# Kernel optimization log

Hardware: AMD Instinct MI355X
Metric: run time of the kernel (lower is better)

The kernel has to match this reference:

```python
import jax, jax.numpy as jnp
import numpy as np

B, S, H = 2, 2048, 2048
NH, NKV, HD = 16, 8, 128        # head_dim = H // NH
WINDOW = 1024                    # sliding window size
THETA = 100000.0                 # rope_theta (RotaryEmbedding base)


def setup_inputs() -> dict:
    key = jax.random.key(0)
    ks = jax.random.split(key, 5)
    hidden = jax.random.normal(ks[0], (B, S, H), jnp.float32)
    # fused QKV projection: [H, NH*HD + 2*NKV*HD]
    W_pack = jax.random.normal(ks[1], (H, NH * HD + 2 * NKV * HD), jnp.float32) * (H ** -0.5)
    W_o = jax.random.normal(ks[2], (NH * HD, H), jnp.float32) * ((NH * HD) ** -0.5)
    # per-KV-head 2-tap causal conv weights, softmax-normalized (as in nn.Parameter init)
    conv_k = jax.nn.softmax(jax.random.normal(ks[3], (NKV, 2), jnp.float32), axis=-1)
    conv_v = jax.nn.softmax(jax.random.normal(ks[4], (NKV, 2), jnp.float32), axis=-1)
    return {"hidden": hidden, "W_pack": W_pack, "W_o": W_o, "conv_k": conv_k, "conv_v": conv_v}


def _rope(x, cos, sin):
    # x: (b, s, h, d); cos/sin: (s, d//2); non-interleaved (rotate-half) form
    d2 = x.shape[-1] // 2
    x1, x2 = x[..., :d2], x[..., d2:]
    c = cos[None, :, None, :]
    s = sin[None, :, None, :]
    return jnp.concatenate([x1 * c - x2 * s, x2 * c + x1 * s], axis=-1)


def _causal_conv2(x, w):
    # x: (b, s, kv, d); w: (kv, 2). out[t] = w0*x[t-1] + w1*x[t], zero-padded at t=0
    x_prev = jnp.pad(x, ((0, 0), (1, 0), (0, 0), (0, 0)))[:, :-1]
    return w[None, None, :, 0:1] * x_prev + w[None, None, :, 1:2] * x


def reference(hidden, W_pack, W_o, conv_k, conv_v):
    b, s, _ = hidden.shape
    qkv = hidden @ W_pack                                  # (b, s, NH*HD + 2*NKV*HD)
    q = qkv[..., : NH * HD].reshape(b, s, NH, HD)
    k = qkv[..., NH * HD : NH * HD + NKV * HD].reshape(b, s, NKV, HD)
    v = qkv[..., NH * HD + NKV * HD :].reshape(b, s, NKV, HD)

    inv_freq = 1.0 / (THETA ** (jnp.arange(0, HD, 2, dtype=jnp.float32) / HD))
    freqs = jnp.outer(jnp.arange(s, dtype=jnp.float32), inv_freq)  # (s, HD/2)
    cos, sin = jnp.cos(freqs), jnp.sin(freqs)
    q = _rope(q, cos, sin)
    k = _rope(k, cos, sin)

    # learned 2-tap causal conv mixing adjacent K/V states, per KV head
    k = _causal_conv2(k, conv_k)
    v = _causal_conv2(v, conv_v)

    # GQA: repeat kv heads to match query heads
    group = NH // NKV
    k = jnp.repeat(k, group, axis=2)  # (b, s, NH, HD)
    v = jnp.repeat(v, group, axis=2)

    scores = jnp.einsum('bqhd,bkhd->bhqk', q, k) / jnp.sqrt(jnp.float32(HD))
    i = jnp.arange(s)[:, None]
    j = jnp.arange(s)[None, :]
    mask = (j <= i) & (i - j < WINDOW)  # causal sliding-window mask
    scores = jnp.where(mask[None, None], scores, jnp.finfo(scores.dtype).min)
    probs = jax.nn.softmax(scores, axis=-1)
    out = jnp.einsum('bhqk,bkhd->bqhd', probs, v).reshape(b, s, NH * HD)
    return out @ W_o
```

## Files before the change

kernel.cpp:

```cpp
#include <hip/hip_runtime.h>

#define DI __device__ __forceinline__

typedef unsigned short u16;
typedef __attribute__((ext_vector_type(8))) short s16x8;
typedef __attribute__((ext_vector_type(8))) unsigned short u16x8;
typedef __attribute__((ext_vector_type(4))) float f32x4;
typedef __attribute__((ext_vector_type(16))) float f32x16;

DI u16 f2bf(float x) {
  union { float f; unsigned u; } a; a.f = x;
  unsigned r = a.u + 0x7FFFu + ((a.u >> 16) & 1u);
  return (u16)(r >> 16);
}
DI float bf2f(u16 u) {
  union { unsigned u; float f; } a; a.u = ((unsigned)u) << 16;
  return a.f;
}
DI void gload16(const void* g, void* l) {
  __builtin_amdgcn_global_load_lds(
      (const __attribute__((address_space(1))) unsigned int*)g,
      (__attribute__((address_space(3))) unsigned int*)l, 16, 0, 0);
}
DI f32x4 mfma16(s16x8 a, s16x8 b, f32x4 c) {
  return __builtin_amdgcn_mfma_f32_16x16x32_bf16(a, b, c, 0, 0, 0);
}
DI f32x16 mfma32(s16x8 a, s16x8 b, f32x16 c) {
  return __builtin_amdgcn_mfma_f32_32x32x16_bf16(a, b, c, 0, 0, 0);
}

DI void store4(u16* p, f32x4 v) {
  union { u16 u[4]; unsigned long long ll; } o;
  o.u[0] = f2bf(v[0]); o.u[1] = f2bf(v[1]); o.u[2] = f2bf(v[2]); o.u[3] = f2bf(v[3]);
  *(unsigned long long*)p = o.ll;
}
DI void store4(float* p, f32x4 v) { *(f32x4*)p = v; }

#define SBAR() asm volatile("s_barrier" ::: "memory")

__global__ void cvt_kernel(const float* __restrict__ in, u16* __restrict__ out, int n8) {
  int i = blockIdx.x * 256 + threadIdx.x;
  if (i >= n8) return;
  const float4* p = (const float4*)in + (size_t)i * 2;
  float4 a = p[0], b = p[1];
  u16x8 o;
  o[0] = f2bf(a.x); o[1] = f2bf(a.y); o[2] = f2bf(a.z); o[3] = f2bf(a.w);
  o[4] = f2bf(b.x); o[5] = f2bf(b.y); o[6] = f2bf(b.z); o[7] = f2bf(b.w);
  *((u16x8*)out + i) = o;
}

__global__ void cvt_t_kernel(const float* __restrict__ W, u16* __restrict__ Wt, int R, int C) {
  __shared__ u16 tile[64][65];
  int c0 = blockIdx.x * 64, r0 = blockIdx.y * 64;
  int t = threadIdx.x;
#pragma unroll
  for (int i = 0; i < 16; ++i) {
    int flat = i * 256 + t;
    int r = flat >> 6, c = flat & 63;
    tile[r][c] = f2bf(W[(size_t)(r0 + r) * C + (c0 + c)]);
  }
  __syncthreads();
#pragma unroll
  for (int i = 0; i < 16; ++i) {
    int flat = i * 256 + t;
    int c = flat >> 6, r = flat & 63;
    Wt[(size_t)(c0 + c) * R + (r0 + r)] = tile[r][c];
  }
}

__global__ void rope_table_kernel(float* __restrict__ cosT, float* __restrict__ sinT) {
  int i = blockIdx.x * 256 + threadIdx.x;
  int s = i >> 6, d = i & 63;
  float inv = expf(-(float)d * (11.5129254649702295f / 64.f));
  float f = (float)s * inv;
  cosT[i] = cosf(f);
  sinT[i] = sinf(f);
}

template <typename OutT>
__global__ __launch_bounds__(512, 2) void gemm8p_kernel(
    const u16* __restrict__ A, const u16* __restrict__ Bt, OutT* __restrict__ C,
    int M, int N, int K) {
  __shared__ __align__(16) char lds[131072];
  int nwg = gridDim.x;
  int bid = blockIdx.x;
  int cpx = nwg >> 3;
  int swz = (bid & 7) * cpx + (bid >> 3);
  int ntn = N >> 8;
  int bm = swz / ntn, bn = swz - bm * ntn;
  int m0 = bm << 8, n0 = bn << 8;
  int t = threadIdx.x, w = t >> 6, l = t & 63;
  int wm = w >> 2, wn = w & 3;
  int NT = K >> 6;

  unsigned offA[2][2], offB[2][2];
  int cA[2][2], cB[2][2];
#pragma unroll
  for (int h = 0; h < 2; ++h)
#pragma unroll
    for (int i = 0; i < 2; ++i) {
      int c = i * 16 + h * 8 + w;
      cA[h][i] = c;
      int d = c * 1024 + l * 16;
      int s = d ^ ((((d >> 7) & 7)) << 4);
      offA[h][i] = (unsigned)(m0 + (s >> 7)) * (unsigned)(K * 2) + (unsigned)(s & 127);
      int c2 = ((w >> 2) << 3) + (w & 3) + h * 4 + i * 16;
      cB[h][i] = c2;
      int d2 = c2 * 1024 + l * 16;
      int s2 = d2 ^ ((((d2 >> 7) & 7)) << 4);
      offB[h][i] = (unsigned)(n0 + (s2 >> 7)) * (unsigned)(K * 2) + (unsigned)(s2 & 127);
    }
  const char* Ab = (const char*)A;
  const char* Bb = (const char*)Bt;

#define STAGE_A(tile, h) do { int _t = (tile); if (_t < NT) {                  \
    unsigned _k = (unsigned)_t * 128u;                                          \
    char* _ba = lds + ((_t & 1) << 16);                                         \
    gload16(Ab + (size_t)(offA[h][0] + _k), _ba + cA[h][0] * 1024);             \
    gload16(Ab + (size_t)(offA[h][1] + _k), _ba + cA[h][1] * 1024); } } while (0)
#define STAGE_B(tile, h) do { int _t = (tile); if (_t < NT) {                  \
    unsigned _k = (unsigned)_t * 128u;                                          \
    char* _bb = lds + ((_t & 1) << 16) + 32768;                                 \
    gload16(Bb + (size_t)(offB[h][0] + _k), _bb + cB[h][0] * 1024);             \
    gload16(Bb + (size_t)(offB[h][1] + _k), _bb + cB[h][1] * 1024); } } while (0)

  int lanemix = ((l & 15) << 7) + ((((l >> 4) << 4) ^ ((l & 7) << 4)));
  int lanemix1 = lanemix ^ 64;

  f32x4 acc[8][4] = {};
  s16x8 af[4][2], b0f[2][2], b1f[2][2];

  STAGE_A(0, 0); STAGE_B(0, 0); STAGE_A(0, 1); STAGE_B(0, 1);
  STAGE_A(1, 0); STAGE_B(1, 0); STAGE_A(1, 1);
  asm volatile("s_waitcnt vmcnt(6)" ::: "memory");
  SBAR();

  for (int tt = 0; tt < NT; ++tt) {
    const char* ldsA = lds + ((tt & 1) << 16);
    const char* ldsB = ldsA + 32768;
    const char* Ard0 = ldsA + (wm << 14) + lanemix;
    const char* Ard1 = ldsA + (wm << 14) + lanemix1;
    const char* Brd0 = ldsB + (wn << 13) + lanemix;
    const char* Brd1 = ldsB + (wn << 13) + lanemix1;

#pragma unroll
    for (int mf = 0; mf < 4; ++mf) {
      af[mf][0] = *(const s16x8*)(Ard0 + mf * 2048);
      af[mf][1] = *(const s16x8*)(Ard1 + mf * 2048);
    }
#pragma unroll
    for (int nf = 0; nf < 2; ++nf) {
      b0f[nf][0] = *(const s16x8*)(Brd0 + nf * 2048);
      b0f[nf][1] = *(const s16x8*)(Brd1 + nf * 2048);
    }
    STAGE_B(tt + 1, 1);
    SBAR();
    __builtin_amdgcn_s_setprio(1);
#pragma unroll
    for (int mf = 0; mf < 4; ++mf)
#pragma unroll
      for (int nf = 0; nf < 2; ++nf) {
        acc[mf][nf] = mfma16(b0f[nf][0], af[mf][0], acc[mf][nf]);
        acc[mf][nf] = mfma16(b0f[nf][1], af[mf][1], acc[mf][nf]);
      }
    __builtin_amdgcn_s_setprio(0);
    SBAR();

#pragma unroll
    for (int nf = 0; nf < 2; ++nf) {
      b1f[nf][0] = *(const s16x8*)(Brd0 + (nf + 2) * 2048);
      b1f[nf][1] = *(const s16x8*)(Brd1 + (nf + 2) * 2048);
    }
    STAGE_A(tt + 2, 0);
    SBAR();
    __builtin_amdgcn_s_setprio(1);
#pragma unroll
    for (int mf = 0; mf < 4; ++mf)
#pragma unroll
      for (int nf = 0; nf < 2; ++nf) {
        acc[mf][nf + 2] = mfma16(b1f[nf][0], af[mf][0], acc[mf][nf + 2]);
        acc[mf][nf + 2] = mfma16(b1f[nf][1], af[mf][1], acc[mf][nf + 2]);
      }
    __builtin_amdgcn_s_setprio(0);
    SBAR();

#pragma unroll
    for (int mf = 0; mf < 4; ++mf) {
      af[mf][0] = *(const s16x8*)(Ard0 + (mf + 4) * 2048);
      af[mf][1] = *(const s16x8*)(Ard1 + (mf + 4) * 2048);
    }
    STAGE_B(tt + 2, 0);
    SBAR();
    __builtin_amdgcn_s_setprio(1);
#pragma unroll
    for (int mf = 0; mf < 4; ++mf)
#pragma unroll
      for (int nf = 0; nf < 2; ++nf) {
        acc[mf + 4][nf] = mfma16(b0f[nf][0], af[mf][0], acc[mf + 4][nf]);
        acc[mf + 4][nf] = mfma16(b0f[nf][1], af[mf][1], acc[mf + 4][nf]);
      }
    __builtin_amdgcn_s_setprio(0);
    SBAR();

    STAGE_A(tt + 2, 1);
    SBAR();
    __builtin_amdgcn_s_setprio(1);
#pragma unroll
    for (int mf = 0; mf < 4; ++mf)
#pragma unroll
      for (int nf = 0; nf < 2; ++nf) {
        acc[mf + 4][nf + 2] = mfma16(b1f[nf][0], af[mf][0], acc[mf + 4][nf + 2]);
        acc[mf + 4][nf + 2] = mfma16(b1f[nf][1], af[mf][1], acc[mf + 4][nf + 2]);
      }
    __builtin_amdgcn_s_setprio(0);
    if (tt < NT - 2) asm volatile("s_waitcnt vmcnt(6)" ::: "memory");
    else             asm volatile("s_waitcnt vmcnt(0)" ::: "memory");
    SBAR();
  }
#undef STAGE_A
#undef STAGE_B

#pragma unroll
  for (int mf = 0; mf < 8; ++mf) {
    int row = m0 + wm * 128 + mf * 16 + (l & 15);
    OutT* crow = C + (size_t)row * N + n0 + wn * 64 + (l >> 4) * 4;
#pragma unroll
    for (int nf = 0; nf < 4; ++nf) store4(crow + nf * 16, acc[mf][nf]);
  }
}

__global__ __launch_bounds__(512, 2) void gemm8pn_kernel(
    const u16* __restrict__ A, const u16* __restrict__ Bt, float* __restrict__ C,
    int M, int N, int K) {
  __shared__ __align__(16) char lds[98304];
  int nwg = gridDim.x;
  int bid = blockIdx.x;
  int cpx = nwg >> 3;
  int swz = (bid & 7) * cpx + (bid >> 3);
  int ntn = N >> 7;
  int bm = swz / ntn, bn = swz - bm * ntn;
  int m0 = bm << 8, n0 = bn << 7;
  int t = threadIdx.x, w = t >> 6, l = t & 63;
  int wm = w >> 2, wn = w & 3;
  int NT = K >> 6;

  unsigned offA[4], offB[2];
  int cA[4], cB[2];
#pragma unroll
  for (int u = 0; u < 4; ++u) {
    int c = u * 8 + w;
    cA[u] = c;
    int d = c * 1024 + l * 16;
    int s = d ^ ((((d >> 7) & 7)) << 4);
    offA[u] = (unsigned)(m0 + (s >> 7)) * (unsigned)(K * 2) + (unsigned)(s & 127);
  }
#pragma unroll
  for (int u = 0; u < 2; ++u) {
    int c = u * 8 + w;
    cB[u] = c;
    int d = c * 1024 + l * 16;
    int s = d ^ ((((d >> 7) & 7)) << 4);
    offB[u] = (unsigned)(n0 + (s >> 7)) * (unsigned)(K * 2) + (unsigned)(s & 127);
  }
  const char* Ab = (const char*)A;
  const char* Bb = (const char*)Bt;

#define STG_A(tile, u) do { int _t = (tile); if (_t < NT) {                    \
    gload16(Ab + (size_t)(offA[u] + (unsigned)_t * 128u),                       \
            lds + (_t & 1) * 49152 + cA[u] * 1024); } } while (0)
#define STG_B(tile, u) do { int _t = (tile); if (_t < NT) {                    \
    gload16(Bb + (size_t)(offB[u] + (unsigned)_t * 128u),                       \
            lds + (_t & 1) * 49152 + 32768 + cB[u] * 1024); } } while (0)

  int lanemix = ((l & 15) << 7) + ((((l >> 4) << 4) ^ ((l & 7) << 4)));
  int lanemix1 = lanemix ^ 64;

  f32x4 acc[8][2] = {};
  s16x8 af[4][2], bf0[2], bf1[2];

  STG_A(0, 0); STG_A(0, 1); STG_A(0, 2); STG_A(0, 3); STG_B(0, 0); STG_B(0, 1);
  STG_A(1, 0); STG_A(1, 1); STG_A(1, 2); STG_A(1, 3); STG_B(1, 0); STG_B(1, 1);
  asm volatile("s_waitcnt vmcnt(6)" ::: "memory");
  SBAR();

  for (int tt = 0; tt < NT; ++tt) {
    const char* ldsA = lds + (tt & 1) * 49152;
    const char* ldsB = ldsA + 32768;
    const char* Ard0 = ldsA + (wm << 14) + lanemix;
    const char* Ard1 = ldsA + (wm << 14) + lanemix1;
    const char* Brd0 = ldsB + (wn << 12) + lanemix;
    const char* Brd1 = ldsB + (wn << 12) + lanemix1;

#pragma unroll
    for (int mf = 0; mf < 4; ++mf) {
      af[mf][0] = *(const s16x8*)(Ard0 + mf * 2048);
      af[mf][1] = *(const s16x8*)(Ard1 + mf * 2048);
    }
    bf0[0] = *(const s16x8*)(Brd0);
    bf0[1] = *(const s16x8*)(Brd1);
    SBAR();
    __builtin_amdgcn_s_setprio(1);
#pragma unroll
    for (int mf = 0; mf < 4; ++mf) {
      acc[mf][0] = mfma16(bf0[0], af[mf][0], acc[mf][0]);
      acc[mf][0] = mfma16(bf0[1], af[mf][1], acc[mf][0]);
    }
    __builtin_amdgcn_s_setprio(0);
    SBAR();

    bf1[0] = *(const s16x8*)(Brd0 + 2048);
    bf1[1] = *(const s16x8*)(Brd1 + 2048);
    STG_A(tt + 2, 0); STG_A(tt + 2, 2);
    SBAR();
    __builtin_amdgcn_s_setprio(1);
#pragma unroll
    for (int mf = 0; mf < 4; ++mf) {
      acc[mf][1] = mfma16(bf1[0], af[mf][0], acc[mf][1]);
      acc[mf][1] = mfma16(bf1[1], af[mf][1], acc[mf][1]);
    }
    __builtin_amdgcn_s_setprio(0);
    SBAR();

#pragma unroll
    for (int mf = 0; mf < 4; ++mf) {
      af[mf][0] = *(const s16x8*)(Ard0 + (mf + 4) * 2048);
      af[mf][1] = *(const s16x8*)(Ard1 + (mf + 4) * 2048);
    }
    STG_B(tt + 2, 0); STG_B(tt + 2, 1);
    SBAR();
    __builtin_amdgcn_s_setprio(1);
#pragma unroll
    for (int mf = 0; mf < 4; ++mf) {
      acc[mf + 4][0] = mfma16(bf0[0], af[mf][0], acc[mf + 4][0]);
      acc[mf + 4][0] = mfma16(bf0[1], af[mf][1], acc[mf + 4][0]);
    }
    __builtin_amdgcn_s_setprio(0);
    SBAR();

    STG_A(tt + 2, 1); STG_A(tt + 2, 3);
    SBAR();
    __builtin_amdgcn_s_setprio(1);
#pragma unroll
    for (int mf = 0; mf < 4; ++mf) {
      acc[mf + 4][1] = mfma16(bf1[0], af[mf][0], acc[mf + 4][1]);
      acc[mf + 4][1] = mfma16(bf1[1], af[mf][1], acc[mf + 4][1]);
    }
    __builtin_amdgcn_s_setprio(0);
    if (tt < NT - 2) asm volatile("s_waitcnt vmcnt(6)" ::: "memory");
    else             asm volatile("s_waitcnt vmcnt(0)" ::: "memory");
    SBAR();
  }
#undef STG_A
#undef STG_B

#pragma unroll
  for (int mf = 0; mf < 8; ++mf) {
    int row = m0 + wm * 128 + mf * 16 + (l & 15);
    float* crow = C + (size_t)row * N + n0 + wn * 32 + (l >> 4) * 4;
#pragma unroll
    for (int nf = 0; nf < 2; ++nf) store4(crow + nf * 16, acc[mf][nf]);
  }
}

__global__ void ropeconv_kernel(const u16* __restrict__ qkv, const float* __restrict__ cosT,
                                const float* __restrict__ sinT, const float* __restrict__ convk,
                                u16* __restrict__ qb, u16* __restrict__ kb) {
  const float qs = 0.08838834764831845f;
  int row = blockIdx.x;
  int b = row >> 11, s = row & 2047;
  int t = threadIdx.x;
  const u16* qr = qkv + (size_t)row * 4096;
  u16* qo = qb + (size_t)row * 2048;
#pragma unroll
  for (int i = 0; i < 4; ++i) {
    int p = i * 256 + t;
    int h = p >> 6, d = p & 63;
    float x1 = bf2f(qr[h * 128 + d]), x2 = bf2f(qr[h * 128 + 64 + d]);
    float c = cosT[s * 64 + d], sn = sinT[s * 64 + d];
    qo[h * 128 + d] = f2bf((x1 * c - x2 * sn) * qs);
    qo[h * 128 + 64 + d] = f2bf((x2 * c + x1 * sn) * qs);
  }
  const u16* kr = qr + 2048;
#pragma unroll
  for (int i = 0; i < 2; ++i) {
    int p = i * 256 + t;
    int h = p >> 6, d = p & 63;
    float c = cosT[s * 64 + d], sn = sinT[s * 64 + d];
    float x1 = bf2f(kr[h * 128 + d]), x2 = bf2f(kr[h * 128 + 64 + d]);
    float r1 = x1 * c - x2 * sn, r2 = x2 * c + x1 * sn;
    float p1 = 0.f, p2 = 0.f;
    if (s > 0) {
      const u16* kp = kr - 4096;
      float cp = cosT[(s - 1) * 64 + d], sp = sinT[(s - 1) * 64 + d];
      float y1 = bf2f(kp[h * 128 + d]), y2 = bf2f(kp[h * 128 + 64 + d]);
      p1 = y1 * cp - y2 * sp;
      p2 = y2 * cp + y1 * sp;
    }
    float w0 = convk[h * 2], w1 = convk[h * 2 + 1];
    size_t o = (((size_t)b * 8 + h) * 2048 + s) * 128;
    kb[o + d] = f2bf(w0 * p1 + w1 * r1);
    kb[o + 64 + d] = f2bf(w0 * p2 + w1 * r2);
  }
}

__global__ void vtrans_kernel(const u16* __restrict__ qkv, const float* __restrict__ convv,
                              u16* __restrict__ vt) {
  __shared__ u16 lt[128][72];
  int st = blockIdx.x, bh = blockIdx.y;
  int b = bh >> 3, h = bh & 7;
  int s0 = st * 64;
  int t = threadIdx.x;
  float w0 = convv[h * 2], w1 = convv[h * 2 + 1];
#pragma unroll
  for (int i = 0; i < 32; ++i) {
    int flat = i * 256 + t;
    int sl = flat >> 7, d = flat & 127;
    int s = s0 + sl;
    int row = b * 2048 + s;
    float x = bf2f(qkv[(size_t)row * 4096 + 3072 + h * 128 + d]);
    float xp = (s > 0) ? bf2f(qkv[(size_t)(row - 1) * 4096 + 3072 + h * 128 + d]) : 0.f;
    lt[d][sl] = f2bf(w0 * xp + w1 * x);
  }
  __syncthreads();
#pragma unroll
  for (int i = 0; i < 32; ++i) {
    int flat = i * 256 + t;
    int d = flat >> 6, sl = flat & 63;
    vt[((size_t)(b * 8 + h) * 128 + d) * 2048 + s0 + sl] = lt[d][sl];
  }
}

__global__ __launch_bounds__(256, 2) void attn2_kernel(
    const u16* __restrict__ qb, const u16* __restrict__ kbuf, const u16* __restrict__ vt,
    u16* __restrict__ ao) {
  __shared__ __align__(16) char lds[65536];
  int qt = blockIdx.x, bh = blockIdx.y;
  int b = bh >> 4, h = bh & 15, kh = h >> 1;
  int t = threadIdx.x, w = t >> 6, l = t & 63;
  int i0 = qt * 128;
  int qbase = i0 + w * 32;
  int lq = l & 31, hi = l >> 5;
  int xorc = (l & 7) << 4;
  const char* Kg = (const char*)(kbuf + (size_t)(b * 8 + kh) * 2048 * 128);
  const char* Vg = (const char*)(vt + (size_t)(b * 8 + kh) * 128 * 2048);

  s16x8 qf[8];
  {
    const u16* qp = qb + ((size_t)(b * 2048 + qbase + lq)) * 2048 + h * 128 + 8 * hi;
#pragma unroll
    for (int kc = 0; kc < 8; ++kc) qf[kc] = *(const s16x8*)(qp + kc * 16);
  }

  unsigned ksrc[4], vsrc[4], kdst[4], vdst[4];
#pragma unroll
  for (int i = 0; i < 4; ++i) {
    int c = w * 4 + i;
    int row = c * 4 + (l >> 4);
    int colb = (l & 15) * 16;
    ksrc[i] = (unsigned)(row * 256 + (colb ^ ((row & 7) << 4)));
    kdst[i] = (unsigned)(c * 1024);
    int d = c * 8 + (l >> 3);
    int cb2 = (l & 7) * 16;
    vsrc[i] = (unsigned)(d * 4096 + (cb2 ^ ((d & 7) << 4)));
    vdst[i] = (unsigned)(16384 + c * 1024);
  }

#define STAGEKV(tile, buf) do { int _j2 = (tile) << 6;                          \
    char* _lb = lds + ((buf) << 15);                                             \
    const char* _ks = Kg + (size_t)_j2 * 256;                                    \
    const char* _vs = Vg + (size_t)_j2 * 2;                                      \
    gload16(_ks + ksrc[0], _lb + kdst[0]); gload16(_vs + vsrc[0], _lb + vdst[0]);\
    gload16(_ks + ksrc[1], _lb + kdst[1]); gload16(_vs + vsrc[1], _lb + vdst[1]);\
    gload16(_ks + ksrc[2], _lb + kdst[2]); gload16(_vs + vsrc[2], _lb + vdst[2]);\
    gload16(_ks + ksrc[3], _lb + kdst[3]); gload16(_vs + vsrc[3], _lb + vdst[3]);\
  } while (0)

  int lo = i0 - 1023; if (lo < 0) lo = 0;
  int tk0 = lo >> 6, tk1 = (i0 + 127) >> 6;

  f32x16 acco[4] = {};
  float ls0 = 0.f, ls1 = 0.f, ls2 = 0.f, ls3 = 0.f;

  int cur = 0;
  STAGEKV(tk0, 0);
  asm volatile("s_waitcnt vmcnt(0)" ::: "memory");
  SBAR();

  for (int tk = tk0; tk <= tk1; ++tk) {
    int j0 = tk << 6;
    if (tk < tk1) STAGEKV(tk + 1, cur ^ 1);
    bool relevant = (j0 <= qbase + 31) && (j0 + 63 >= qbase - 1023);
    if (relevant) {
      const char* Kl = lds + (cur << 15);
      const char* Vl = Kl + 16384;
      const char* Krow = Kl + lq * 256;
      f32x16 ps0 = {}, ps1 = {};
      __builtin_amdgcn_s_setprio(1);
#pragma unroll
      for (int kc = 0; kc < 8; ++kc) {
        s16x8 kf = *(const s16x8*)(Krow + ((kc * 32 + hi * 16) ^ xorc));
        ps0 = mfma32(kf, qf[kc], ps0);
      }
#pragma unroll
      for (int kc = 0; kc < 8; ++kc) {
        s16x8 kf = *(const s16x8*)(Krow + 8192 + ((kc * 32 + hi * 16) ^ xorc));
        ps1 = mfma32(kf, qf[kc], ps1);
      }
      __builtin_amdgcn_s_setprio(0);
      bool domask = (j0 + 63 > qbase) || (qbase + 31 - j0 >= 1024);
      int di0 = qbase + lq - j0;
      float pe[32];
#pragma unroll
      for (int r = 0; r < 16; ++r) {
        float s0 = ps0[r], s1 = ps1[r];
        if (domask) {
          int crow = (r & 3) + 8 * (r >> 2) + 4 * hi;
          if ((unsigned)(di0 - crow) >= 1024u) s0 = -1e30f;
          if ((unsigned)(di0 - 32 - crow) >= 1024u) s1 = -1e30f;
        }
        float e0 = __expf(s0), e1 = __expf(s1);
        pe[r] = e0; pe[16 + r] = e1;
        if ((r & 3) == 0) { ls0 += e0 + e1; }
        else if ((r & 3) == 1) { ls1 += e0 + e1; }
        else if ((r & 3) == 2) { ls2 += e0 + e1; }
        else { ls3 += e0 + e1; }
      }
      unsigned pk[16];
#pragma unroll
      for (int p = 0; p < 16; ++p) {
        asm("v_cvt_pk_bf16_f32 %0, %1, %2" : "=v"(pk[p]) : "v"(pe[2 * p]), "v"(pe[2 * p + 1]));
      }
      s16x8 pa[4];
#pragma unroll
      for (int ks = 0; ks < 4; ++ks) {
        int base = (ks >> 1) * 8 + (ks & 1) * 4;
        unsigned keep0 = hi ? pk[base + 2] : pk[base + 0];
        unsigned keep1 = hi ? pk[base + 3] : pk[base + 1];
        unsigned send0 = hi ? pk[base + 0] : pk[base + 2];
        unsigned send1 = hi ? pk[base + 1] : pk[base + 3];
        unsigned recv0 = (unsigned)__shfl_xor((int)send0, 32);
        unsigned recv1 = (unsigned)__shfl_xor((int)send1, 32);
        union { unsigned u[4]; s16x8 v; } pu;
        pu.u[0] = hi ? recv0 : keep0;
        pu.u[1] = hi ? recv1 : keep1;
        pu.u[2] = hi ? keep0 : recv0;
        pu.u[3] = hi ? keep1 : recv1;
        pa[ks] = pu.v;
      }
      __builtin_amdgcn_s_setprio(1);
#pragma unroll
      for (int db = 0; db < 4; ++db) {
        const char* Vrow = Vl + db * 4096 + lq * 128;
#pragma unroll
        for (int ks = 0; ks < 4; ++ks) {
          s16x8 vf = *(const s16x8*)(Vrow + ((ks * 32 + hi * 16) ^ xorc));
          acco[db] = mfma32(pa[ks], vf, acco[db]);
        }
      }
      __builtin_amdgcn_s_setprio(0);
    }
    asm volatile("s_waitcnt vmcnt(0)" ::: "memory");
    SBAR();
    cur ^= 1;
  }
#undef STAGEKV

  float lrow = (ls0 + ls1) + (ls2 + ls3);
  float lt2 = lrow + __shfl_xor(lrow, 32);
  float rinv = 1.f / lt2;
#pragma unroll
  for (int r = 0; r < 16; ++r) {
    int qidx = (r & 3) + 8 * (r >> 2) + 4 * hi;
    float rv = __shfl(rinv, qidx);
    int i = qbase + qidx;
    u16* orow = ao + ((size_t)(b * 2048 + i)) * 2048 + h * 128 + lq;
#pragma unroll
    for (int db = 0; db < 4; ++db)
      orow[db * 32] = f2bf(acco[db][r] * rv);
  }
}

extern "C" void kernel_launch(void* const* d_in, const int* in_sizes, int n_in,
                              void* d_out, int out_size, void* d_ws, size_t ws_size,
                              hipStream_t stream) {
  (void)in_sizes; (void)n_in; (void)out_size; (void)ws_size;
  const float* hidden = (const float*)d_in[0];
  const float* W_pack = (const float*)d_in[1];
  const float* W_o    = (const float*)d_in[2];
  const float* conv_k = (const float*)d_in[3];
  const float* conv_v = (const float*)d_in[4];

  char* ws = (char*)d_ws;
  const size_t MB = 1u << 20;
  u16* hA    = (u16*)(ws + 0);
  u16* wpT   = (u16*)(ws + 16 * MB);
  u16* woT   = (u16*)(ws + 32 * MB);
  u16* qkv   = (u16*)(ws + 40 * MB);
  u16* qb    = (u16*)(ws + 72 * MB);
  u16* kbuf  = (u16*)(ws + 88 * MB);
  u16* vtb   = (u16*)(ws + 96 * MB);
  float* cosT = (float*)(ws + 104 * MB);
  float* sinT = (float*)(ws + 104 * MB + 524288);
  u16* attnb = qkv;

  cvt_kernel<<<4096, 256, 0, stream>>>(hidden, hA, 1048576);
  cvt_t_kernel<<<dim3(64, 32), 256, 0, stream>>>(W_pack, wpT, 2048, 4096);
  cvt_t_kernel<<<dim3(32, 32), 256, 0, stream>>>(W_o, woT, 2048, 2048);
  rope_table_kernel<<<512, 256, 0, stream>>>(cosT, sinT);
  gemm8p_kernel<u16><<<256, 512, 0, stream>>>(hA, wpT, qkv, 4096, 4096, 2048);
  ropeconv_kernel<<<4096, 256, 0, stream>>>(qkv, cosT, sinT, conv_k, qb, kbuf);
  vtrans_kernel<<<dim3(32, 16), 256, 0, stream>>>(qkv, conv_v, vtb);
  attn2_kernel<<<dim3(16, 32), 256, 0, stream>>>(qb, kbuf, vtb, attnb);
  gemm8pn_kernel<<<256, 512, 0, stream>>>(attnb, woT, (float*)d_out,
                                          4096, 2048, 2048);
}
```

Measured before the change: 205.9 us.

## Merge prep and rope/vtrans kernels; switch QKV GEMM to 32x32 MFMA

Four preprocessing launches (hidden convert, two weight transposes, rope table) become one prep_kernel that picks its task from the block index. ropeconv and vtrans likewise become one rcvt_kernel. The QKV projection GEMM's inner loop now uses 32x32x16 bf16 MFMA with a new LDS read swizzle and a matching epilogue, replacing the 16x16x32 fragments. This removes launch gaps and cuts MFMA instruction count, but risks LDS bank conflicts or errors from the new swizzle and fragment layout.

Result: faster. 196.1 us (-4.8%).

```diff
diff --git a/kernel.cpp b/kernel.cpp
--- a/kernel.cpp
+++ b/kernel.cpp
@@ -38,43 +38,53 @@
 
 #define SBAR() asm volatile("s_barrier" ::: "memory")
 
-__global__ void cvt_kernel(const float* __restrict__ in, u16* __restrict__ out, int n8) {
-  int i = blockIdx.x * 256 + threadIdx.x;
-  if (i >= n8) return;
-  const float4* p = (const float4*)in + (size_t)i * 2;
-  float4 a = p[0], b = p[1];
-  u16x8 o;
-  o[0] = f2bf(a.x); o[1] = f2bf(a.y); o[2] = f2bf(a.z); o[3] = f2bf(a.w);
-  o[4] = f2bf(b.x); o[5] = f2bf(b.y); o[6] = f2bf(b.z); o[7] = f2bf(b.w);
-  *((u16x8*)out + i) = o;
-}
-
-__global__ void cvt_t_kernel(const float* __restrict__ W, u16* __restrict__ Wt, int R, int C) {
-  __shared__ u16 tile[64][65];
-  int c0 = blockIdx.x * 64, r0 = blockIdx.y * 64;
+__global__ __launch_bounds__(256) void prep_kernel(
+    const float* __restrict__ hidden, const float* __restrict__ W_pack,
+    const float* __restrict__ W_o, u16* __restrict__ hA, u16* __restrict__ wpT,
+    u16* __restrict__ woT, float* __restrict__ cosT, float* __restrict__ sinT) {
+  int bi = blockIdx.x;
   int t = threadIdx.x;
-#pragma unroll
-  for (int i = 0; i < 16; ++i) {
-    int flat = i * 256 + t;
-    int r = flat >> 6, c = flat & 63;
-    tile[r][c] = f2bf(W[(size_t)(r0 + r) * C + (c0 + c)]);
-  }
-  __syncthreads();
-#pragma unroll
-  for (int i = 0; i < 16; ++i) {
-    int flat = i * 256 + t;
-    int c = flat >> 6, r = flat & 63;
-    Wt[(size_t)(c0 + c) * R + (r0 + r)] = tile[r][c];
-  }
-}
-
-__global__ void rope_table_kernel(float* __restrict__ cosT, float* __restrict__ sinT) {
-  int i = blockIdx.x * 256 + threadIdx.x;
-  int s = i >> 6, d = i & 63;
-  float inv = expf(-(float)d * (11.5129254649702295f / 64.f));
-  float f = (float)s * inv;
-  cosT[i] = cosf(f);
-  sinT[i] = sinf(f);
+  if (bi < 4096) {
+    int i = bi * 256 + t;
+    const float4* p = (const float4*)hidden + (size_t)i * 2;
+    float4 a = p[0], b = p[1];
+    u16x8 o;
+    o[0] = f2bf(a.x); o[1] = f2bf(a.y); o[2] = f2bf(a.z); o[3] = f2bf(a.w);
+    o[4] = f2bf(b.x); o[5] = f2bf(b.y); o[6] = f2bf(b.z); o[7] = f2bf(b.w);
+    *((u16x8*)hA + i) = o;
+  } else if (bi < 7168) {
+    const float* W; u16* Wt; int R, C, c0, r0;
+    if (bi < 6144) {
+      int idx = bi - 4096;
+      W = W_pack; Wt = wpT; R = 2048; C = 4096;
+      c0 = (idx & 63) * 64; r0 = (idx >> 6) * 64;
+    } else {
+      int idx = bi - 6144;
+      W = W_o; Wt = woT; R = 2048; C = 2048;
+      c0 = (idx & 31) * 64; r0 = (idx >> 5) * 64;
+    }
+    __shared__ u16 tile[64][65];
+#pragma unroll
+    for (int i = 0; i < 16; ++i) {
+      int flat = i * 256 + t;
+      int r = flat >> 6, c = flat & 63;
+      tile[r][c] = f2bf(W[(size_t)(r0 + r) * C + (c0 + c)]);
+    }
+    __syncthreads();
+#pragma unroll
+    for (int i = 0; i < 16; ++i) {
+      int flat = i * 256 + t;
+      int c = flat >> 6, r = flat & 63;
+      Wt[(size_t)(c0 + c) * R + (r0 + r)] = tile[r][c];
+    }
+  } else {
+    int i = (bi - 7168) * 256 + t;
+    int s = i >> 6, d = i & 63;
+    float inv = expf(-(float)d * (11.5129254649702295f / 64.f));
+    float f = (float)s * inv;
+    cosT[i] = cosf(f);
+    sinT[i] = sinf(f);
+  }
 }
 
 template <typename OutT>
@@ -124,11 +134,12 @@
     gload16(Bb + (size_t)(offB[h][0] + _k), _bb + cB[h][0] * 1024);             \
     gload16(Bb + (size_t)(offB[h][1] + _k), _bb + cB[h][1] * 1024); } } while (0)
 
-  int lanemix = ((l & 15) << 7) + ((((l >> 4) << 4) ^ ((l & 7) << 4)));
-  int lanemix1 = lanemix ^ 64;
-
-  f32x4 acc[8][4] = {};
-  s16x8 af[4][2], b0f[2][2], b1f[2][2];
+  int hi = l >> 5;
+  int rowb = (l & 31) << 7;
+  unsigned lmix = (((unsigned)(l & 7) << 4) ^ ((unsigned)hi << 4));
+
+  f32x16 acc[4][2] = {};
+  s16x8 af[2][4], bf0[4], bf1[4];
 
   STAGE_A(0, 0); STAGE_B(0, 0); STAGE_A(0, 1); STAGE_B(0, 1);
   STAGE_A(1, 0); STAGE_B(1, 0); STAGE_A(1, 1);
@@ -138,67 +149,55 @@
   for (int tt = 0; tt < NT; ++tt) {
     const char* ldsA = lds + ((tt & 1) << 16);
     const char* ldsB = ldsA + 32768;
-    const char* Ard0 = ldsA + (wm << 14) + lanemix;
-    const char* Ard1 = ldsA + (wm << 14) + lanemix1;
-    const char* Brd0 = ldsB + (wn << 13) + lanemix;
-    const char* Brd1 = ldsB + (wn << 13) + lanemix1;
-
-#pragma unroll
-    for (int mf = 0; mf < 4; ++mf) {
-      af[mf][0] = *(const s16x8*)(Ard0 + mf * 2048);
-      af[mf][1] = *(const s16x8*)(Ard1 + mf * 2048);
-    }
-#pragma unroll
-    for (int nf = 0; nf < 2; ++nf) {
-      b0f[nf][0] = *(const s16x8*)(Brd0 + nf * 2048);
-      b0f[nf][1] = *(const s16x8*)(Brd1 + nf * 2048);
-    }
+    const char* Ard = ldsA + (wm << 14) + rowb;
+    const char* Brd = ldsB + (wn << 13) + rowb;
+
+#pragma unroll
+    for (int mb = 0; mb < 2; ++mb)
+#pragma unroll
+      for (int kc = 0; kc < 4; ++kc)
+        af[mb][kc] = *(const s16x8*)(Ard + mb * 4096 + (lmix ^ (unsigned)(kc << 5)));
+#pragma unroll
+    for (int kc = 0; kc < 4; ++kc)
+      bf0[kc] = *(const s16x8*)(Brd + (lmix ^ (unsigned)(kc << 5)));
     STAGE_B(tt + 1, 1);
     SBAR();
     __builtin_amdgcn_s_setprio(1);
 #pragma unroll
-    for (int mf = 0; mf < 4; ++mf)
-#pragma unroll
-      for (int nf = 0; nf < 2; ++nf) {
-        acc[mf][nf] = mfma16(b0f[nf][0], af[mf][0], acc[mf][nf]);
-        acc[mf][nf] = mfma16(b0f[nf][1], af[mf][1], acc[mf][nf]);
-      }
-    __builtin_amdgcn_s_setprio(0);
-    SBAR();
-
-#pragma unroll
-    for (int nf = 0; nf < 2; ++nf) {
-      b1f[nf][0] = *(const s16x8*)(Brd0 + (nf + 2) * 2048);
-      b1f[nf][1] = *(const s16x8*)(Brd1 + (nf + 2) * 2048);
-    }
+    for (int kc = 0; kc < 4; ++kc) {
+      acc[0][0] = mfma32(bf0[kc], af[0][kc], acc[0][0]);
+      acc[1][0] = mfma32(bf0[kc], af[1][kc], acc[1][0]);
+    }
+    __builtin_amdgcn_s_setprio(0);
+    SBAR();
+
+#pragma unroll
+    for (int kc = 0; kc < 4; ++kc)
+      bf1[kc] = *(const s16x8*)(Brd + 4096 + (lmix ^ (unsigned)(kc << 5)));
     STAGE_A(tt + 2, 0);
     SBAR();
     __builtin_amdgcn_s_setprio(1);
 #pragma unroll
-    for (int mf = 0; mf < 4; ++mf)
-#pragma unroll
-      for (int nf = 0; nf < 2; ++nf) {
-        acc[mf][nf + 2] = mfma16(b1f[nf][0], af[mf][0], acc[mf][nf + 2]);
-        acc[mf][nf + 2] = mfma16(b1f[nf][1], af[mf][1], acc[mf][nf + 2]);
-      }
-    __builtin_amdgcn_s_setprio(0);
-    SBAR();
-
-#pragma unroll
-    for (int mf = 0; mf < 4; ++mf) {
-      af[mf][0] = *(const s16x8*)(Ard0 + (mf + 4) * 2048);
-      af[mf][1] = *(const s16x8*)(Ard1 + (mf + 4) * 2048);
-    }
+    for (int kc = 0; kc < 4; ++kc) {
+      acc[0][1] = mfma32(bf1[kc], af[0][kc], acc[0][1]);
+      acc[1][1] = mfma32(bf1[kc], af[1][kc], acc[1][1]);
+    }
+    __builtin_amdgcn_s_setprio(0);
+    SBAR();
+
+#pragma unroll
+    for (int mb = 0; mb < 2; ++mb)
+#pragma unroll
+      for (int kc = 0; kc < 4; ++kc)
+        af[mb][kc] = *(const s16x8*)(Ard + 8192 + mb * 4096 + (lmix ^ (unsigned)(kc << 5)));
     STAGE_B(tt + 2, 0);
     SBAR();
     __builtin_amdgcn_s_setprio(1);
 #pragma unroll
-    for (int mf = 0; mf < 4; ++mf)
-#pragma unroll
-      for (int nf = 0; nf < 2; ++nf) {
-        acc[mf + 4][nf] = mfma16(b0f[nf][0], af[mf][0], acc[mf + 4][nf]);
-        acc[mf + 4][nf] = mfma16(b0f[nf][1], af[mf][1], acc[mf + 4][nf]);
-      }
+    for (int kc = 0; kc < 4; ++kc) {
+      acc[2][0] = mfma32(bf0[kc], af[0][kc], acc[2][0]);
+      acc[3][0] = mfma32(bf0[kc], af[1][kc], acc[3][0]);
+    }
     __builtin_amdgcn_s_setprio(0);
     SBAR();
 
@@ -206,12 +205,10 @@
     SBAR();
     __builtin_amdgcn_s_setprio(1);
 #pragma unroll
-    for (int mf = 0; mf < 4; ++mf)
-#pragma unroll
-      for (int nf = 0; nf < 2; ++nf) {
-        acc[mf + 4][nf + 2] = mfma16(b1f[nf][0], af[mf][0], acc[mf + 4][nf + 2]);
-        acc[mf + 4][nf + 2] = mfma16(b1f[nf][1], af[mf][1], acc[mf + 4][nf + 2]);
-      }
+    for (int kc = 0; kc < 4; ++kc) {
+      acc[2][1] = mfma32(bf1[kc], af[0][kc], acc[2][1]);
+      acc[3][1] = mfma32(bf1[kc], af[1][kc], acc[3][1]);
+    }
     __builtin_amdgcn_s_setprio(0);
     if (tt < NT - 2) asm volatile("s_waitcnt vmcnt(6)" ::: "memory");
     else             asm volatile("s_waitcnt vmcnt(0)" ::: "memory");
@@ -221,11 +218,18 @@
 #undef STAGE_B
 
 #pragma unroll
-  for (int mf = 0; mf < 8; ++mf) {
-    int row = m0 + wm * 128 + mf * 16 + (l & 15);
-    OutT* crow = C + (size_t)row * N + n0 + wn * 64 + (l >> 4) * 4;
-#pragma unroll
-    for (int nf = 0; nf < 4; ++nf) store4(crow + nf * 16, acc[mf][nf]);
+  for (int mb = 0; mb < 4; ++mb) {
+    int row = m0 + wm * 128 + mb * 32 + (l & 31);
+#pragma unroll
+    for (int nb = 0; nb < 2; ++nb) {
+      OutT* crow = C + (size_t)row * N + n0 + wn * 64 + nb * 32 + 4 * hi;
+      f32x16 v = acc[mb][nb];
+#pragma unroll
+      for (int g = 0; g < 4; ++g) {
+        f32x4 sv = { v[4 * g], v[4 * g + 1], v[4 * g + 2], v[4 * g + 3] };
+        store4(crow + g * 8, sv);
+      }
+    }
   }
 }
 
@@ -362,71 +366,72 @@
   }
 }
 
-__global__ void ropeconv_kernel(const u16* __restrict__ qkv, const float* __restrict__ cosT,
-                                const float* __restrict__ sinT, const float* __restrict__ convk,
-                                u16* __restrict__ qb, u16* __restrict__ kb) {
-  const float qs = 0.08838834764831845f;
-  int row = blockIdx.x;
-  int b = row >> 11, s = row & 2047;
+__global__ void rcvt_kernel(const u16* __restrict__ qkv, const float* __restrict__ cosT,
+                            const float* __restrict__ sinT, const float* __restrict__ convk,
+                            const float* __restrict__ convv,
+                            u16* __restrict__ qb, u16* __restrict__ kb,
+                            u16* __restrict__ vt) {
   int t = threadIdx.x;
-  const u16* qr = qkv + (size_t)row * 4096;
-  u16* qo = qb + (size_t)row * 2048;
-#pragma unroll
-  for (int i = 0; i < 4; ++i) {
-    int p = i * 256 + t;
-    int h = p >> 6, d = p & 63;
-    float x1 = bf2f(qr[h * 128 + d]), x2 = bf2f(qr[h * 128 + 64 + d]);
-    float c = cosT[s * 64 + d], sn = sinT[s * 64 + d];
-    qo[h * 128 + d] = f2bf((x1 * c - x2 * sn) * qs);
-    qo[h * 128 + 64 + d] = f2bf((x2 * c + x1 * sn) * qs);
-  }
-  const u16* kr = qr + 2048;
-#pragma unroll
-  for (int i = 0; i < 2; ++i) {
-    int p = i * 256 + t;
-    int h = p >> 6, d = p & 63;
-    float c = cosT[s * 64 + d], sn = sinT[s * 64 + d];
-    float x1 = bf2f(kr[h * 128 + d]), x2 = bf2f(kr[h * 128 + 64 + d]);
-    float r1 = x1 * c - x2 * sn, r2 = x2 * c + x1 * sn;
-    float p1 = 0.f, p2 = 0.f;
-    if (s > 0) {
-      const u16* kp = kr - 4096;
-      float cp = cosT[(s - 1) * 64 + d], sp = sinT[(s - 1) * 64 + d];
-      float y1 = bf2f(kp[h * 128 + d]), y2 = bf2f(kp[h * 128 + 64 + d]);
-      p1 = y1 * cp - y2 * sp;
-      p2 = y2 * cp + y1 * sp;
-    }
-    float w0 = convk[h * 2], w1 = convk[h * 2 + 1];
-    size_t o = (((size_t)b * 8 + h) * 2048 + s) * 128;
-    kb[o + d] = f2bf(w0 * p1 + w1 * r1);
-    kb[o + 64 + d] = f2bf(w0 * p2 + w1 * r2);
-  }
-}
-
-__global__ void vtrans_kernel(const u16* __restrict__ qkv, const float* __restrict__ convv,
-                              u16* __restrict__ vt) {
-  __shared__ u16 lt[128][72];
-  int st = blockIdx.x, bh = blockIdx.y;
-  int b = bh >> 3, h = bh & 7;
-  int s0 = st * 64;
-  int t = threadIdx.x;
-  float w0 = convv[h * 2], w1 = convv[h * 2 + 1];
-#pragma unroll
-  for (int i = 0; i < 32; ++i) {
-    int flat = i * 256 + t;
-    int sl = flat >> 7, d = flat & 127;
-    int s = s0 + sl;
-    int row = b * 2048 + s;
-    float x = bf2f(qkv[(size_t)row * 4096 + 3072 + h * 128 + d]);
-    float xp = (s > 0) ? bf2f(qkv[(size_t)(row - 1) * 4096 + 3072 + h * 128 + d]) : 0.f;
-    lt[d][sl] = f2bf(w0 * xp + w1 * x);
-  }
-  __syncthreads();
-#pragma unroll
-  for (int i = 0; i < 32; ++i) {
-    int flat = i * 256 + t;
-    int d = flat >> 6, sl = flat & 63;
-    vt[((size_t)(b * 8 + h) * 128 + d) * 2048 + s0 + sl] = lt[d][sl];
+  if (blockIdx.x < 4096) {
+    const float qs = 0.08838834764831845f;
+    int row = blockIdx.x;
+    int b = row >> 11, s = row & 2047;
+    const u16* qr = qkv + (size_t)row * 4096;
+    u16* qo = qb + (size_t)row * 2048;
+#pragma unroll
+    for (int i = 0; i < 4; ++i) {
+      int p = i * 256 + t;
+      int h = p >> 6, d = p & 63;
+      float x1 = bf2f(qr[h * 128 + d]), x2 = bf2f(qr[h * 128 + 64 + d]);
+      float c = cosT[s * 64 + d], sn = sinT[s * 64 + d];
+      qo[h * 128 + d] = f2bf((x1 * c - x2 * sn) * qs);
+      qo[h * 128 + 64 + d] = f2bf((x2 * c + x1 * sn) * qs);
+    }
+    const u16* kr = qr + 2048;
+#pragma unroll
+    for (int i = 0; i < 2; ++i) {
+      int p = i * 256 + t;
+      int h = p >> 6, d = p & 63;
+      float c = cosT[s * 64 + d], sn = sinT[s * 64 + d];
+      float x1 = bf2f(kr[h * 128 + d]), x2 = bf2f(kr[h * 128 + 64 + d]);
+      float r1 = x1 * c - x2 * sn, r2 = x2 * c + x1 * sn;
+      float p1 = 0.f, p2 = 0.f;
+      if (s > 0) {
+        const u16* kp = kr - 4096;
+        float cp = cosT[(s - 1) * 64 + d], sp = sinT[(s - 1) * 64 + d];
+        float y1 = bf2f(kp[h * 128 + d]), y2 = bf2f(kp[h * 128 + 64 + d]);
+        p1 = y1 * cp - y2 * sp;
+        p2 = y2 * cp + y1 * sp;
+      }
+      float w0 = convk[h * 2], w1 = convk[h * 2 + 1];
+      size_t o = (((size_t)b * 8 + h) * 2048 + s) * 128;
+      kb[o + d] = f2bf(w0 * p1 + w1 * r1);
+      kb[o + 64 + d] = f2bf(w0 * p2 + w1 * r2);
+    }
+  } else {
+    __shared__ u16 lt[128][72];
+    int idx = blockIdx.x - 4096;
+    int st = idx & 31, bh = idx >> 5;
+    int b = bh >> 3, h = bh & 7;
+    int s0 = st * 64;
+    float w0 = convv[h * 2], w1 = convv[h * 2 + 1];
+#pragma unroll
+    for (int i = 0; i < 32; ++i) {
+      int flat = i * 256 + t;
+      int sl = flat >> 7, d = flat & 127;
+      int s = s0 + sl;
+      int row = b * 2048 + s;
+      float x = bf2f(qkv[(size_t)row * 4096 + 3072 + h * 128 + d]);
+      float xp = (s > 0) ? bf2f(qkv[(size_t)(row - 1) * 4096 + 3072 + h * 128 + d]) : 0.f;
+      lt[d][sl] = f2bf(w0 * xp + w1 * x);
+    }
+    __syncthreads();
+#pragma unroll
+    for (int i = 0; i < 32; ++i) {
+      int flat = i * 256 + t;
+      int d = flat >> 6, sl = flat & 63;
+      vt[((size_t)(b * 8 + h) * 128 + d) * 2048 + s0 + sl] = lt[d][sl];
+    }
   }
 }
 
@@ -603,13 +608,9 @@
   float* sinT = (float*)(ws + 104 * MB + 524288);
   u16* attnb = qkv;
 
-  cvt_kernel<<<4096, 256, 0, stream>>>(hidden, hA, 1048576);
-  cvt_t_kernel<<<dim3(64, 32), 256, 0, stream>>>(W_pack, wpT, 2048, 4096);
-  cvt_t_kernel<<<dim3(32, 32), 256, 0, stream>>>(W_o, woT, 2048, 2048);
-  rope_table_kernel<<<512, 256, 0, stream>>>(cosT, sinT);
+  prep_kernel<<<7680, 256, 0, stream>>>(hidden, W_pack, W_o, hA, wpT, woT, cosT, sinT);
   gemm8p_kernel<u16><<<256, 512, 0, stream>>>(hA, wpT, qkv, 4096, 4096, 2048);
-  ropeconv_kernel<<<4096, 256, 0, stream>>>(qkv, cosT, sinT, conv_k, qb, kbuf);
-  vtrans_kernel<<<dim3(32, 16), 256, 0, stream>>>(qkv, conv_v, vtb);
+  rcvt_kernel<<<4608, 256, 0, stream>>>(qkv, cosT, sinT, conv_k, conv_v, qb, kbuf, vtb);
   attn2_kernel<<<dim3(16, 32), 256, 0, stream>>>(qb, kbuf, vtb, attnb);
   gemm8pn_kernel<<<256, 512, 0, stream>>>(attnb, woT, (float*)d_out,
                                           4096, 2048, 2048);
```
